# Kernel optimization log

Measured on AMD Instinct MI355X. Metric: run time of the kernel, lower is better.

Reference implementation:

```python
import jax, jax.numpy as jnp
import numpy as np

B, T, U, V = 8, 128, 64, 512  # batch, enc frames, label length, vocab
U1 = U + 1
BLANK = 0


def setup_inputs() -> dict:
    key = jax.random.key(0)
    k1, k2, k3, k4, k5 = jax.random.split(key, 5)
    trans_acts = jax.random.normal(k1, (B, T, V), jnp.float32)
    pred_acts = jax.random.normal(k2, (B, U1, V), jnp.float32)
    labels = jax.random.randint(k3, (B, U), 1, V).astype(jnp.int32)  # 0 is blank
    act_lens = jax.random.randint(k4, (B,), T // 2, T + 1).astype(jnp.int32)
    label_lens = jax.random.randint(k5, (B,), U // 2, U + 1).astype(jnp.int32)
    return dict(trans_acts=trans_acts, pred_acts=pred_acts, labels=labels,
                act_lens=act_lens, label_lens=label_lens)


def _rnnt_costs(trans_acts, pred_acts, labels, act_lens, label_lens, blank=BLANK):
    # joint log-probs: log_softmax(trans[t] + pred[u]) over vocab -> (B,T,U1,V)
    logits = trans_acts[:, :, None, :] + pred_acts[:, None, :, :]
    logp = jax.nn.log_softmax(logits, axis=-1)
    lp_blank = logp[..., blank]                                    # (B,T,U1)
    # label emission log-prob at (t,u): prob of labels[b,u]        # (B,T,U)
    lp_lab = jnp.take_along_axis(
        logp[:, :, :U, :], labels[:, None, :, None].astype(jnp.int32), axis=-1)[..., 0]

    nb, nu1 = trans_acts.shape[0], pred_acts.shape[1]
    # alpha at t=0: alpha[0,u] = sum_{u'<u} lp_lab[0,u']
    alpha0 = jnp.concatenate(
        [jnp.zeros((nb, 1), logp.dtype), jnp.cumsum(lp_lab[:, 0, :], axis=-1)], axis=1)

    def t_step(alpha_prev, xs):
        blank_prev, lab_cur = xs                 # (B,U1), (B,U)
        a_in = alpha_prev + blank_prev           # vertical (blank) transition

        def u_step(carry, x):
            a, d = x                             # a:(B,) from blank path, d:(B,) label lp
            new = jnp.logaddexp(a, carry + d)
            return new, new

        _, rest = jax.lax.scan(u_step, a_in[:, 0], (a_in[:, 1:].T, lab_cur.T))
        alpha_t = jnp.concatenate([a_in[:, :1], rest.T], axis=1)
        return alpha_t, alpha_t

    xs = (jnp.swapaxes(lp_blank[:, :-1, :], 0, 1),   # blank lp at t-1: (T-1,B,U1)
          jnp.swapaxes(lp_lab[:, 1:, :], 0, 1))      # label lp at t:  (T-1,B,U)
    _, alphas = jax.lax.scan(t_step, alpha0, xs)     # (T-1,B,U1)
    alphas = jnp.concatenate([alpha0[None], alphas], axis=0)  # (T,B,U1)

    b_idx = jnp.arange(nb)
    t_idx = act_lens - 1
    u_idx = label_lens
    ll = alphas[t_idx, b_idx, u_idx] + lp_blank[b_idx, t_idx, u_idx]
    return -ll                                       # per-example cost (B,)


def reference(trans_acts, pred_acts, labels, act_lens, label_lens):
    costs = _rnnt_costs(trans_acts, pred_acts, labels, act_lens, label_lens)
    # size_average=False: return summed cost as a length-1 vector (as torch FloatTensor([sum]))
    return jnp.sum(costs)[None]
```

## Files before the change

kernel.cpp:

```cpp
#include <hip/hip_runtime.h>
#include <math.h>

#define Bn 8
#define Tn 128
#define Un 64
#define U1n 65
#define Vn 512
#define NEG (-1e30f)
#define LOG2E 1.4426950408889634f
#define LN2 0.6931471805599453f
#define VP 516

template <int CTRL>
__device__ __forceinline__ float dpp_mv(float x) {
  return __int_as_float(__builtin_amdgcn_update_dpp(
      __float_as_int(x), __float_as_int(x), CTRL, 0xF, 0xF, false));
}

__device__ __forceinline__ float red_sum64(float m) {
  m += dpp_mv<0xB1>(m);
  m += dpp_mv<0x4E>(m);
  m += dpp_mv<0x141>(m);
  m += dpp_mv<0x140>(m);
  m += __shfl_xor(m, 16);
  m += __shfl_xor(m, 32);
  return m;
}

__device__ __forceinline__ float wave_shr1_fill(float x, float fill) {
  return __int_as_float(__builtin_amdgcn_update_dpp(
      __float_as_int(fill), __float_as_int(x), 0x138, 0xF, 0xF, false));
}

__device__ __forceinline__ float hw_exp2(float x) {
  return __builtin_amdgcn_exp2f(x);
}
__device__ __forceinline__ float hw_log2(float x) {
  return __builtin_amdgcn_logf(x);
}

__device__ __forceinline__ float laddexp2(float a, float b) {
  float mx = fmaxf(a, b), mn = fminf(a, b);
  return mx + hw_log2(1.f + hw_exp2(mn - mx));
}

__global__ __launch_bounds__(256) void rnnt_dots(
    const float* __restrict__ trans, const float* __restrict__ pred,
    const int* __restrict__ labels, float* __restrict__ lbT,
    float* __restrict__ llT, float* __restrict__ out) {
  __shared__ float EPs[U1n * VP];
  __shared__ float ETs[4 * VP];
  __shared__ float pr0s[U1n];
  __shared__ float prls[Un];
  __shared__ int lbls[Un];

  if (blockIdx.x == 0 && threadIdx.x == 0) out[0] = 0.f;

  int b = blockIdx.x >> 5;
  int chunk = blockIdx.x & 31;
  int tid = threadIdx.x;
  int w = tid >> 6;
  int lane = tid & 63;
  int t = chunk * 4 + w;

  if (tid < U1n) {
    pr0s[tid] = pred[((size_t)b * U1n + tid) * Vn];
    if (tid < Un) {
      int lbl = labels[b * Un + tid];
      lbls[tid] = lbl;
      prls[tid] = pred[((size_t)b * U1n + tid) * Vn + lbl];
    }
  }

  const float4* pred4 = (const float4*)(pred + (size_t)b * U1n * Vn);
#pragma unroll
  for (int k = 0; k < 33; ++k) {
    int idx = tid + k * 256;
    if (idx < U1n * 128) {
      int u = idx >> 7, j = idx & 127;
      float4 pv = pred4[u * 128 + j];
      float4 ev;
      ev.x = hw_exp2(pv.x * LOG2E);
      ev.y = hw_exp2(pv.y * LOG2E);
      ev.z = hw_exp2(pv.z * LOG2E);
      ev.w = hw_exp2(pv.w * LOG2E);
      *(float4*)&EPs[u * VP + j * 4] = ev;
    }
  }

  const float* trow = trans + ((size_t)b * Tn + t) * Vn;
  const float4* trow4 = (const float4*)trow;
  {
    float4 x0 = trow4[lane], x1 = trow4[lane + 64];
    float4 e0, e1;
    e0.x = hw_exp2(x0.x * LOG2E); e0.y = hw_exp2(x0.y * LOG2E);
    e0.z = hw_exp2(x0.z * LOG2E); e0.w = hw_exp2(x0.w * LOG2E);
    e1.x = hw_exp2(x1.x * LOG2E); e1.y = hw_exp2(x1.y * LOG2E);
    e1.z = hw_exp2(x1.z * LOG2E); e1.w = hw_exp2(x1.w * LOG2E);
    *(float4*)&ETs[w * VP + lane * 8] = e0;
    *(float4*)&ETs[w * VP + lane * 8 + 4] = e1;
  }
  __syncthreads();

  int u = lane;
  float ac0 = 0.f, ac1 = 0.f, ac2 = 0.f, ac3 = 0.f;
  int epb = u * VP, etb = w * VP;
#pragma unroll 4
  for (int vc = 0; vc < Vn; vc += 4) {
    float4 ep = *(const float4*)&EPs[epb + vc];
    float4 et = *(const float4*)&ETs[etb + vc];
    ac0 += et.x * ep.x;
    ac1 += et.y * ep.y;
    ac2 += et.z * ep.z;
    ac3 += et.w * ep.w;
  }
  float dot = (ac0 + ac2) + (ac1 + ac3);

  float p64;
  {
    float4 eA = *(const float4*)&EPs[64 * VP + lane * 8];
    float4 eB = *(const float4*)&EPs[64 * VP + lane * 8 + 4];
    float4 tA = *(const float4*)&ETs[etb + lane * 8];
    float4 tB = *(const float4*)&ETs[etb + lane * 8 + 4];
    float part = eA.x * tA.x + eA.y * tA.y + eA.z * tA.z + eA.w * tA.w +
                 eB.x * tB.x + eB.y * tB.y + eB.z * tB.z + eB.w * tB.w;
    p64 = red_sum64(part);
  }

  float tr0v = trow[0];
  float lse2 = hw_log2(dot);
  lbT[((size_t)b * U1n + u) * Tn + t] = (tr0v + pr0s[u]) * LOG2E - lse2;
  float trl = trow[lbls[u]];
  llT[((size_t)b * Un + u) * Tn + t] = (trl + prls[u]) * LOG2E - lse2;
  if (lane == 0) {
    lbT[((size_t)b * U1n + 64) * Tn + t] =
        (tr0v + pr0s[64]) * LOG2E - hw_log2(p64);
  }
}

__global__ __launch_bounds__(64) void rnnt_alpha(
    const float* __restrict__ lbT, const float* __restrict__ llT,
    const int* __restrict__ act_lens, const int* __restrict__ label_lens,
    float* __restrict__ out) {
  int b = blockIdx.x;
  int l = threadIdx.x;

  const float* LBrow = lbT + ((size_t)b * U1n + l + 1) * Tn;
  const float* LLrow = llT + ((size_t)b * Un + l) * Tn;
  const float* L0row = lbT + (size_t)b * U1n * Tn;

  int ti = act_lens[b] - 1;
  int ui = label_lens[b];
  int s_end = ti + ui;
  bool is_rec = (l == ui - 1);

  float a = NEG, p = 0.f, rec = 0.f;
  float lbB[8], llB[8], l0B[8];
#pragma unroll
  for (int k = 0; k < 8; ++k) {
    lbB[k] = LBrow[k - l - 1];
    llB[k] = LLrow[k - l];
    l0B[k] = L0row[k];
  }

  for (int sb = 0; sb < s_end; sb += 8) {
#pragma unroll
    for (int k = 0; k < 8; ++k) {
      int s = sb + k;
      float lb_t = lbB[k], ll_t = llB[k], l0_t = l0B[k];
      lbB[k] = LBrow[s + 8 - l - 1];
      llB[k] = LLrow[s + 8 - l];
      l0B[k] = L0row[s + 8];

      float nb = wave_shr1_fill(a, p);
      float vert = a + lb_t;
      float horiz = nb + ll_t;
      float an = laddexp2(vert, horiz);
      int t = s - l;
      a = (t >= 0) ? an : NEG;
      p += l0_t;
      if ((t == ti) & is_rec) rec = an;
    }
  }

  float r = __shfl(rec, ui - 1);
  if (l == 0) {
    float lbv = lbT[((size_t)b * U1n + ui) * Tn + ti];
    atomicAdd(out, -(r + lbv) * LN2);
  }
}

extern "C" void kernel_launch(void* const* d_in, const int* in_sizes, int n_in,
                              void* d_out, int out_size, void* d_ws, size_t ws_size,
                              hipStream_t stream) {
  const float* trans = (const float*)d_in[0];
  const float* pred = (const float*)d_in[1];
  const int* labels = (const int*)d_in[2];
  const int* act_lens = (const int*)d_in[3];
  const int* label_lens = (const int*)d_in[4];
  float* out = (float*)d_out;

  float* lbT = (float*)d_ws + 64;
  float* llT = lbT + Bn * U1n * Tn;

  rnnt_dots<<<Bn * 32, 256, 0, stream>>>(trans, pred, labels, lbT, llT, out);
  rnnt_alpha<<<Bn, 64, 0, stream>>>(lbT, llT, act_lens, label_lens, out);
}
```

Before: 26.05 us.

## Store joint log-probs in anti-diagonal layout for coalesced alpha loads

The dots kernel now writes blank and label log-probs into a diagonal-major buffer indexed by (t+u, u), with a separate array for the u=0 blank row. In the alpha wavefront kernel, each diagonal step's loads become contiguous across lanes, replacing the strided per-lane row reads of the old layout. The cost moves to scattered, uncoalesced writes in the dots kernel. It also relies on unwritten padding and NEG sentinel cells so that lanes ahead of the wavefront read harmless values.

```diff
diff --git a/kernel.cpp b/kernel.cpp
--- a/kernel.cpp
+++ b/kernel.cpp
@@ -10,6 +10,8 @@
 #define LOG2E 1.4426950408889634f
 #define LN2 0.6931471805599453f
 #define VP 516
+#define SROWS 208
+#define SDSZ (SROWS * 64)
 
 template <int CTRL>
 __device__ __forceinline__ float dpp_mv(float x) {
@@ -46,8 +48,9 @@
 
 __global__ __launch_bounds__(256) void rnnt_dots(
     const float* __restrict__ trans, const float* __restrict__ pred,
-    const int* __restrict__ labels, float* __restrict__ lbT,
-    float* __restrict__ llT, float* __restrict__ out) {
+    const int* __restrict__ labels, float* __restrict__ lbD,
+    float* __restrict__ llD, float* __restrict__ l0D,
+    float* __restrict__ out) {
   __shared__ float EPs[U1n * VP];
   __shared__ float ETs[4 * VP];
   __shared__ float pr0s[U1n];
@@ -129,25 +132,31 @@
 
   float tr0v = trow[0];
   float lse2 = hw_log2(dot);
-  lbT[((size_t)b * U1n + u) * Tn + t] = (tr0v + pr0s[u]) * LOG2E - lse2;
-  float trl = trow[lbls[u]];
-  llT[((size_t)b * Un + u) * Tn + t] = (trl + prls[u]) * LOG2E - lse2;
+  float lbv = (tr0v + pr0s[u]) * LOG2E - lse2;
+  float llv = (trow[lbls[u]] + prls[u]) * LOG2E - lse2;
+
+  float* lbDb = lbD + (size_t)b * SDSZ;
+  float* llDb = llD + (size_t)b * SDSZ;
   if (lane == 0) {
-    lbT[((size_t)b * U1n + 64) * Tn + t] =
-        (tr0v + pr0s[64]) * LOG2E - hw_log2(p64);
-  }
+    l0D[b * 256 + t] = lbv;
+    lbDb[(t + 64) * 64 + 63] = (tr0v + pr0s[64]) * LOG2E - hw_log2(p64);
+  } else {
+    lbDb[(t + lane) * 64 + (lane - 1)] = lbv;
+  }
+  llDb[(t + lane) * 64 + lane] = llv;
+  if (t == 0) lbDb[lane * 64 + lane] = NEG;
 }
 
 __global__ __launch_bounds__(64) void rnnt_alpha(
-    const float* __restrict__ lbT, const float* __restrict__ llT,
-    const int* __restrict__ act_lens, const int* __restrict__ label_lens,
-    float* __restrict__ out) {
+    const float* __restrict__ lbD, const float* __restrict__ llD,
+    const float* __restrict__ l0D, const int* __restrict__ act_lens,
+    const int* __restrict__ label_lens, float* __restrict__ out) {
   int b = blockIdx.x;
   int l = threadIdx.x;
 
-  const float* LBrow = lbT + ((size_t)b * U1n + l + 1) * Tn;
-  const float* LLrow = llT + ((size_t)b * Un + l) * Tn;
-  const float* L0row = lbT + (size_t)b * U1n * Tn;
+  const float* LBd = lbD + (size_t)b * SDSZ;
+  const float* LLd = llD + (size_t)b * SDSZ;
+  const float* L0d = l0D + b * 256;
 
   int ti = act_lens[b] - 1;
   int ui = label_lens[b];
@@ -158,9 +167,9 @@
   float lbB[8], llB[8], l0B[8];
 #pragma unroll
   for (int k = 0; k < 8; ++k) {
-    lbB[k] = LBrow[k - l - 1];
-    llB[k] = LLrow[k - l];
-    l0B[k] = L0row[k];
+    lbB[k] = LBd[k * 64 + l];
+    llB[k] = LLd[k * 64 + l];
+    l0B[k] = L0d[k];
   }
 
   for (int sb = 0; sb < s_end; sb += 8) {
@@ -168,9 +177,9 @@
     for (int k = 0; k < 8; ++k) {
       int s = sb + k;
       float lb_t = lbB[k], ll_t = llB[k], l0_t = l0B[k];
-      lbB[k] = LBrow[s + 8 - l - 1];
-      llB[k] = LLrow[s + 8 - l];
-      l0B[k] = L0row[s + 8];
+      lbB[k] = LBd[(s + 8) * 64 + l];
+      llB[k] = LLd[(s + 8) * 64 + l];
+      l0B[k] = L0d[s + 8];
 
       float nb = wave_shr1_fill(a, p);
       float vert = a + lb_t;
@@ -185,7 +194,7 @@
 
   float r = __shfl(rec, ui - 1);
   if (l == 0) {
-    float lbv = lbT[((size_t)b * U1n + ui) * Tn + ti];
+    float lbv = LBd[s_end * 64 + (ui - 1)];
     atomicAdd(out, -(r + lbv) * LN2);
   }
 }
@@ -200,9 +209,11 @@
   const int* label_lens = (const int*)d_in[4];
   float* out = (float*)d_out;
 
-  float* lbT = (float*)d_ws + 64;
-  float* llT = lbT + Bn * U1n * Tn;
-
-  rnnt_dots<<<Bn * 32, 256, 0, stream>>>(trans, pred, labels, lbT, llT, out);
-  rnnt_alpha<<<Bn, 64, 0, stream>>>(lbT, llT, act_lens, label_lens, out);
-}
+  float* lbD = (float*)d_ws;
+  float* llD = lbD + Bn * SDSZ;
+  float* l0D = llD + Bn * SDSZ;
+
+  rnnt_dots<<<Bn * 32, 256, 0, stream>>>(trans, pred, labels, lbD, llD, l0D,
+                                         out);
+  rnnt_alpha<<<Bn, 64, 0, stream>>>(lbD, llD, l0D, act_lens, label_lens, out);
+}
```

After: 27.49 us. 1.06x slower.
